# Kernel optimization log

Hardware: AMD Instinct MI355X
Metric: run time of the kernel (lower is better)

The kernel has to match this reference:

```python
import jax, jax.numpy as jnp
import numpy as np

B, S, E, H, VS, VT = 128, 256, 512, 512, 32000, 32000


def _lstm_layer(x, mask, Wih, Whh, bih, bhh):
    # x: (S,B,E_in), mask: (S,B) bool. PyTorch gate order i,f,g,o.
    h0 = jnp.zeros((x.shape[1], Whh.shape[1]), x.dtype)
    c0 = h0
    def step(carry, inp):
        h, c = carry
        xt, mt = inp
        g = xt @ Wih.T + h @ Whh.T + bih + bhh
        i, f, gg, o = jnp.split(g, 4, axis=-1)
        i = jax.nn.sigmoid(i); f = jax.nn.sigmoid(f)
        gg = jnp.tanh(gg); o = jax.nn.sigmoid(o)
        c_new = f * c + i * gg
        h_new = o * jnp.tanh(c_new)
        m = mt[:, None]
        h2 = jnp.where(m, h_new, h)
        c2 = jnp.where(m, c_new, c)
        return (h2, c2), jnp.where(m, h_new, 0.0)  # pad_packed zero-pads
    (hT, cT), ys = jax.lax.scan(step, (h0, c0), (x, mask))
    return ys, cT


def setup_inputs() -> dict:
    key = jax.random.key(0)
    ks = jax.random.split(key, 32)
    def w(k, shape, fan_in):
        bound = 1.0 / np.sqrt(fan_in)
        return jax.random.uniform(k, shape, jnp.float32, -bound, bound)
    src_tokens = jax.random.randint(ks[0], (B, S), 0, VS)
    src_lens = jnp.sort(jax.random.randint(ks[1], (B,), S // 2, S + 1))[::-1]
    src_lens = src_lens.at[0].set(S)  # pack_padded expects descending, max = S
    trg_tokens = jax.random.randint(ks[2], (B,), 0, VT)
    inp = {
        'src_tokens': src_tokens, 'src_lens': src_lens, 'trg_tokens': trg_tokens,
        'src_emb': jax.random.normal(ks[3], (VS, E), jnp.float32),
        'trg_emb': jax.random.normal(ks[4], (VT, E), jnp.float32),
        'enc_Wih0': w(ks[5], (4 * H, E), H), 'enc_Whh0': w(ks[6], (4 * H, H), H),
        'enc_bih0': w(ks[7], (4 * H,), H), 'enc_bhh0': w(ks[8], (4 * H,), H),
        'enc_Wih1': w(ks[9], (4 * H, H), H), 'enc_Whh1': w(ks[10], (4 * H, H), H),
        'enc_bih1': w(ks[11], (4 * H,), H), 'enc_bhh1': w(ks[12], (4 * H,), H),
        'dec_Wih': w(ks[13], (4 * H, E + H), H), 'dec_Whh': w(ks[14], (4 * H, H), H),
        'dec_bih': w(ks[15], (4 * H,), H), 'dec_bhh': w(ks[16], (4 * H,), H),
        'W_init': w(ks[17], (H, 2 * H), 2 * H), 'b_init': w(ks[18], (H,), 2 * H),
        'W_hid': w(ks[19], (H, 2 * H), 2 * H), 'b_hid': w(ks[20], (H,), 2 * H),
        'W_out': w(ks[21], (VT, H), H), 'b_out': w(ks[22], (VT,), H),
    }
    return inp


def reference(src_tokens, src_lens, trg_tokens, src_emb, trg_emb,
              enc_Wih0, enc_Whh0, enc_bih0, enc_bhh0,
              enc_Wih1, enc_Whh1, enc_bih1, enc_bhh1,
              dec_Wih, dec_Whh, dec_bih, dec_bhh,
              W_init, b_init, W_hid, b_hid, W_out, b_out):
    # ---- encode ----
    x = src_emb[src_tokens]                       # (B,S,E)
    x = jnp.transpose(x, (1, 0, 2))               # (S,B,E)
    mask = jnp.arange(S)[:, None] < src_lens[None, :]  # (S,B)
    y0, c0f = _lstm_layer(x, mask, enc_Wih0, enc_Whh0, enc_bih0, enc_bhh0)
    y1, c1f = _lstm_layer(y0, mask, enc_Wih1, enc_Whh1, enc_bih1, enc_bhh1)
    src_states = jnp.transpose(y1, (1, 0, 2))     # (B,S,H)
    # final cell states (num_layers,B,H) -> (B, num_layers*H)
    final_cells = jnp.concatenate([c0f, c1f], axis=-1)  # (B,2H)
    c_dec = final_cells @ W_init.T + b_init       # (B,H)
    h_dec = jnp.tanh(c_dec)
    # ---- one decoder step ----
    emb_t = trg_emb[trg_tokens]                   # (B,E)
    vec = jnp.concatenate([emb_t, jnp.zeros((B, H), emb_t.dtype)], axis=-1)
    g = vec @ dec_Wih.T + h_dec @ dec_Whh.T + dec_bih + dec_bhh
    i, f, gg, o = jnp.split(g, 4, axis=-1)
    c = jax.nn.sigmoid(f) * c_dec + jax.nn.sigmoid(i) * jnp.tanh(gg)
    h = jax.nn.sigmoid(o) * jnp.tanh(c)           # (B,H)
    # ---- masked dot attention ----
    scores = jnp.einsum('bsh,bh->bs', src_states, h)
    smask = jnp.arange(S)[None, :] < src_lens[:, None]
    scores = jnp.where(smask, scores, -jnp.inf)
    attw = jax.nn.softmax(scores, axis=-1)
    context = jnp.einsum('bs,bsh->bh', attw, src_states)
    attn_vec = jnp.concatenate([h, context], axis=-1) @ W_hid.T + b_hid
    logits = attn_vec @ W_out.T + b_out
    prd_token = jnp.argmax(logits, axis=-1)       # softmax is monotone
    return context, h, prd_token
```

## Files before the change

kernel.cpp:

```cpp
#include <hip/hip_runtime.h>
#include <stdint.h>


typedef _Float16 f16;
typedef f16 f16x8 __attribute__((ext_vector_type(8)));
typedef float f32x4 __attribute__((ext_vector_type(4)));

#define LOSCALE 2048.0f
#define LOINV   (1.0f/2048.0f)

#define B_  128
#define S_  256
#define H_  512

__device__ __forceinline__ uint16_t hbits(f16 h){ union{ f16 f; uint16_t u; } c; c.f=h; return c.u; }

__device__ __forceinline__ uint32_t split_ph2(float x){
  f16 h = (f16)x;
  float r = (x - (float)h) * LOSCALE;
  return (uint32_t)hbits(h) | ((uint32_t)hbits((f16)r) << 16);
}
__device__ __forceinline__ float ph2val(uint32_t p){
  union{ uint16_t u; f16 f; } a, b; a.u = (uint16_t)p; b.u = (uint16_t)(p>>16);
  return (float)a.f + (float)b.f * LOINV;
}

__device__ __forceinline__ void pack_hi_lo(const uint4& a, const uint4& b, uint4& hi, uint4& lo){
  hi = make_uint4((a.x & 0xffffu) | (a.y << 16),
                  (a.z & 0xffffu) | (a.w << 16),
                  (b.x & 0xffffu) | (b.y << 16),
                  (b.z & 0xffffu) | (b.w << 16));
  lo = make_uint4((a.x >> 16) | (a.y & 0xffff0000u),
                  (a.z >> 16) | (a.w & 0xffff0000u),
                  (b.x >> 16) | (b.y & 0xffff0000u),
                  (b.z >> 16) | (b.w & 0xffff0000u));
}

__device__ __forceinline__ void split_pack8(const float* x, uint4& hi, uint4& lo){
  uint16_t h[8], l[8];
#pragma unroll
  for (int e = 0; e < 8; ++e) {
    f16 hh = (f16)x[e];
    float r = (x[e] - (float)hh) * LOSCALE;
    h[e] = hbits(hh); l[e] = hbits((f16)r);
  }
  hi = make_uint4((uint32_t)h[0]|((uint32_t)h[1]<<16), (uint32_t)h[2]|((uint32_t)h[3]<<16),
                  (uint32_t)h[4]|((uint32_t)h[5]<<16), (uint32_t)h[6]|((uint32_t)h[7]<<16));
  lo = make_uint4((uint32_t)l[0]|((uint32_t)l[1]<<16), (uint32_t)l[2]|((uint32_t)l[3]<<16),
                  (uint32_t)l[4]|((uint32_t)l[5]<<16), (uint32_t)l[6]|((uint32_t)l[7]<<16));
}

__device__ __forceinline__ f32x4 mfma16(uint4 a, uint4 b, f32x4 c){
  return __builtin_amdgcn_mfma_f32_16x16x32_f16(
      __builtin_bit_cast(f16x8, a), __builtin_bit_cast(f16x8, b), c, 0, 0, 0);
}

__device__ __forceinline__ float sigm(float x){ return 1.0f/(1.0f + expf(-x)); }
__device__ __forceinline__ float fsigm(float x){ return 1.0f/(1.0f + __expf(-x)); }
__device__ __forceinline__ float ftanh(float x){
  float ax = fabsf(x);
  float e = __expf(-2.0f*ax);
  float r = (1.0f - e)/(1.0f + e);
  return copysignf(r, x);
}

__device__ __forceinline__ uint32_t plane_word(uint32_t p, uint32_t pp, int odd){
  return odd ? ((pp >> 16) | (p & 0xffff0000u))
             : ((p & 0xffffu) | (pp << 16));
}

__device__ __forceinline__ size_t fl_idx(int row, int k){
  return (size_t)(k >> 5) * 4096 + (size_t)(row >> 4) * 512 + (size_t)(k & 1) * 256
       + (size_t)((k >> 3) & 3) * 64 + (size_t)(row & 15) * 4 + (size_t)((k & 7) >> 1);
}

__device__ __forceinline__ void gload_lds16(const uint32_t* gbase, uint32_t* lbase, int lane){
#if __has_builtin(__builtin_amdgcn_global_load_lds)
  __builtin_amdgcn_global_load_lds(
      (const __attribute__((address_space(1))) uint32_t*)(gbase + lane*4),
      (__attribute__((address_space(3))) uint32_t*)lbase, 16, 0, 0);
#else
  *(uint4*)(lbase + lane*4) = *(const uint4*)(gbase + lane*4);
#endif
}

__global__ __launch_bounds__(256) void k_embed_src_fl(const int* __restrict__ tok,
    const float* __restrict__ emb, uint32_t* __restrict__ out)
{
  const size_t total = (size_t)S_ * B_ * H_;
  for (size_t i = (size_t)blockIdx.x*256 + threadIdx.x; i < total; i += (size_t)gridDim.x*256) {
    int s = (int)(i >> 16), b = (int)((i >> 9) & 127), k = (int)(i & 511);
    int t = tok[b*S_ + s];
    uint32_t p = split_ph2(emb[(size_t)t*H_ + k]);
    uint32_t pp = __shfl_xor(p, 1);
    out[(size_t)s*65536 + fl_idx(b, k)] = plane_word(p, pp, k & 1);
  }
}

__global__ __launch_bounds__(256) void k_embed_trg(const int* __restrict__ tok,
    const float* __restrict__ emb, uint32_t* __restrict__ out)
{
  int i = blockIdx.x*256 + threadIdx.x;
  int e = i & (H_-1), b = i >> 9;
  int t = tok[b];
  out[i] = split_ph2(emb[(size_t)t*H_ + e]);
}

__global__ __launch_bounds__(256) void k_packW(const float* __restrict__ W,
    uint32_t* __restrict__ out)
{
  int i = blockIdx.x*256 + threadIdx.x;
  int n = i >> 9, k = i & 511;
  uint32_t p = split_ph2(W[i]);
  uint32_t pp = __shfl_xor(p, 1);
  out[(size_t)(n >> 7)*65536 + fl_idx(n & 127, k)] = plane_word(p, pp, k & 1);
}

__global__ __launch_bounds__(256) void k_packAfl(const float* __restrict__ a,
    uint32_t* __restrict__ out)
{
  int i = blockIdx.x*256 + threadIdx.x;
  int b = i >> 9, k = i & 511;
  uint32_t p = split_ph2(a[i]);
  uint32_t pp = __shfl_xor(p, 1);
  out[fl_idx(b, k)] = plane_word(p, pp, k & 1);
}

__global__ __launch_bounds__(256,2) void k_gemm_fl(
    const uint32_t* __restrict__ Afl,
    const uint32_t* __restrict__ Wfl,
    const float* __restrict__ b0, const float* __restrict__ b1,
    float* __restrict__ C, int N, int addC)
{
  __shared__ uint8_t sm[65536];
  const int tid = threadIdx.x, lane = tid & 63, wv = tid >> 6;
  const int wm = wv >> 1, wn = wv & 1;
  const int bn0 = blockIdx.x * 128, bm0 = blockIdx.y * 128;
  const uint32_t* Ab = Afl + (size_t)blockIdx.y * 65536;
  const uint32_t* Wb = Wfl + (size_t)blockIdx.x * 65536;

  f32x4 acc0[4][4], acc1[4][4];
#pragma unroll
  for (int i = 0; i < 4; ++i)
#pragma unroll
    for (int j = 0; j < 4; ++j) { acc0[i][j] = (f32x4){0,0,0,0}; acc1[i][j] = (f32x4){0,0,0,0}; }

  for (int it = 0; it < 8; ++it) {
    __syncthreads();
    {
      const uint32_t* gsrc = (wv < 2 ? Ab : Wb) + (size_t)it*8192 + (size_t)(wv & 1)*4096;
      uint32_t* lb = (uint32_t*)(sm + (size_t)wv*16384);
#pragma unroll
      for (int e = 0; e < 16; ++e)
        gload_lds16(gsrc + e*256, lb + e*256, lane);
    }
    asm volatile("s_waitcnt vmcnt(0)" ::: "memory");
    __syncthreads();

#pragma unroll
    for (int kt = 0; kt < 2; ++kt) {
      uint4 ah[4], al[4];
#pragma unroll
      for (int i = 0; i < 4; ++i) {
        const uint8_t* p = sm + (size_t)(kt*8 + wm*4 + i)*2048 + lane*16;
        ah[i] = *(const uint4*)p; al[i] = *(const uint4*)(p + 1024);
      }
#pragma unroll
      for (int j = 0; j < 4; ++j) {
        const uint8_t* p = sm + 32768 + (size_t)(kt*8 + wn*4 + j)*2048 + lane*16;
        uint4 bh = *(const uint4*)p;
        uint4 bl = *(const uint4*)(p + 1024);
#pragma unroll
        for (int i = 0; i < 4; ++i) {
          acc0[i][j] = mfma16(ah[i], bh, acc0[i][j]);
          acc1[i][j] = mfma16(al[i], bh, acc1[i][j]);
          acc1[i][j] = mfma16(ah[i], bl, acc1[i][j]);
        }
      }
    }
  }

#pragma unroll
  for (int i = 0; i < 4; ++i) {
    int row0 = bm0 + (wm*4+i)*16 + ((lane>>4)<<2);
#pragma unroll
    for (int j = 0; j < 4; ++j) {
      int col = bn0 + (wn*4+j)*16 + (lane & 15);
      float bias = 0.f;
      if (b0) bias += b0[col];
      if (b1) bias += b1[col];
      f32x4 v = acc0[i][j] + acc1[i][j] * LOINV;
#pragma unroll
      for (int r = 0; r < 4; ++r) {
        size_t idx = (size_t)(row0 + r) * N + col;
        float out = v[r] + bias;
        if (addC) out += C[idx];
        C[idx] = out;
      }
    }
  }
}

__global__ __launch_bounds__(256,2) void k_gemm(
    const uint32_t* __restrict__ A, int lda,
    const float* __restrict__ W, int ldw,
    const float* __restrict__ b0, const float* __restrict__ b1,
    float* __restrict__ C, int N, int K, int addC)
{
  __shared__ uint8_t sm[65536];
  const int tid = threadIdx.x;
  const int lane = tid & 63, wv = tid >> 6;
  const int wm = wv >> 1, wn = wv & 1;
  const int bn0 = blockIdx.x * 128, bm0 = blockIdx.y * 128;

  const int srow = tid >> 1;
  const int skh  = (tid & 1) * 32;
  const int smt  = srow >> 4, sr = srow & 15, skt = tid & 1;

  f32x4 acc0[4][4], acc1[4][4];
#pragma unroll
  for (int i = 0; i < 4; ++i)
#pragma unroll
    for (int j = 0; j < 4; ++j) { acc0[i][j] = (f32x4){0,0,0,0}; acc1[i][j] = (f32x4){0,0,0,0}; }

  for (int k0 = 0; k0 < K; k0 += 64) {
    __syncthreads();
    {
      const uint32_t* ap = A + (size_t)(bm0 + srow) * lda + (k0 + skh);
      uint4 q[8];
#pragma unroll
      for (int e = 0; e < 8; ++e) q[e] = *(const uint4*)(ap + e*4);
#pragma unroll
      for (int kg = 0; kg < 4; ++kg) {
        uint4 hi, lo; pack_hi_lo(q[2*kg], q[2*kg+1], hi, lo);
        uint8_t* dst = sm + (size_t)(smt*2 + skt)*2048 + (size_t)(sr + 16*kg)*16;
        *(uint4*)dst = hi; *(uint4*)(dst + 1024) = lo;
      }
    }
    {
      const float* wp = W + (size_t)(bn0 + srow) * ldw + (k0 + skh);
      float xs[32];
#pragma unroll
      for (int e = 0; e < 8; ++e) { float4 v = *(const float4*)(wp + e*4);
        xs[e*4+0]=v.x; xs[e*4+1]=v.y; xs[e*4+2]=v.z; xs[e*4+3]=v.w; }
#pragma unroll
      for (int kg = 0; kg < 4; ++kg) {
        uint4 hi, lo; split_pack8(xs + kg*8, hi, lo);
        uint8_t* dst = sm + 32768 + (size_t)(smt*2 + skt)*2048 + (size_t)(sr + 16*kg)*16;
        *(uint4*)dst = hi; *(uint4*)(dst + 1024) = lo;
      }
    }
    __syncthreads();

#pragma unroll
    for (int kt = 0; kt < 2; ++kt) {
      uint4 ah[4], al[4];
#pragma unroll
      for (int i = 0; i < 4; ++i) {
        const uint8_t* p = sm + (size_t)(((wm*4+i)*2 + kt))*2048 + lane*16;
        ah[i] = *(const uint4*)p; al[i] = *(const uint4*)(p + 1024);
      }
#pragma unroll
      for (int j = 0; j < 4; ++j) {
        const uint8_t* p = sm + 32768 + (size_t)(((wn*4+j)*2 + kt))*2048 + lane*16;
        uint4 bh = *(const uint4*)p;
        uint4 bl = *(const uint4*)(p + 1024);
#pragma unroll
        for (int i = 0; i < 4; ++i) {
          acc0[i][j] = mfma16(ah[i], bh, acc0[i][j]);
          acc1[i][j] = mfma16(al[i], bh, acc1[i][j]);
          acc1[i][j] = mfma16(ah[i], bl, acc1[i][j]);
        }
      }
    }
  }

#pragma unroll
  for (int i = 0; i < 4; ++i) {
    int row0 = bm0 + (wm*4+i)*16 + ((lane>>4)<<2);
#pragma unroll
    for (int j = 0; j < 4; ++j) {
      int col = bn0 + (wn*4+j)*16 + (lane & 15);
      float bias = 0.f;
      if (b0) bias += b0[col];
      if (b1) bias += b1[col];
      f32x4 v = acc0[i][j] + acc1[i][j] * LOINV;
#pragma unroll
      for (int r = 0; r < 4; ++r) {
        size_t idx = (size_t)(row0 + r) * N + col;
        float out = v[r] + bias;
        if (addC) out += C[idx];
        C[idx] = out;
      }
    }
  }
}

__global__ __launch_bounds__(256,1) void k_lstm2(
    const float* __restrict__ Whh0, const float* __restrict__ Whh1,
    const float* __restrict__ bih1, const float* __restrict__ bhh1,
    const float* __restrict__ xg,
    const int*  __restrict__ lens,
    uint32_t* __restrict__ mb0,
    uint32_t* __restrict__ mb1,
    float* __restrict__ cb0, float* __restrict__ cb1,
    uint32_t* __restrict__ y1buf,
    uint32_t* __restrict__ flg0, uint32_t* __restrict__ flg1,
    uint32_t* __restrict__ xcdclaim,
    const uint32_t* __restrict__ Wp1,
    int s0, int nt)
{
  __shared__ uint8_t sm[163840];
  uint8_t* wih = sm;
  uint8_t* tile = sm + 131072;
  uint64_t* tile64 = (uint64_t*)tile;
  float* g0ex = (float*)tile;
  float* g1ex = (float*)(tile + 4096);

  const int tid = threadIdx.x, lane = tid & 63, wv = tid >> 6;
  const int row = lane & 15, qh = lane >> 4;

  uint32_t* claim_sh = (uint32_t*)tile;
  if (tid == 0) {
    uint32_t xcd;
    asm volatile("s_getreg_b32 %0, hwreg(HW_REG_XCC_ID)" : "=s"(xcd));
    xcd &= 7u;
    uint32_t pos = __hip_atomic_fetch_add(xcdclaim + xcd*16, 1u,
                     __ATOMIC_RELAXED, __HIP_MEMORY_SCOPE_SYSTEM);
    claim_sh[0] = xcd | ((pos & 31u) << 8);
  }
  __syncthreads();
  const uint32_t cl = claim_sh[0];
  const int bg = (int)(cl & 7u), hs = (int)((cl >> 8) & 31u);
  __syncthreads();

  {
    const uint32_t* wpb = Wp1 + (size_t)(wv*4 + (hs >> 3))*65536 + (size_t)(hs & 7)*512;
    uint32_t* lb = (uint32_t*)(wih + (size_t)wv*32768);
#pragma unroll
    for (int kt = 0; kt < 16; ++kt) {
      gload_lds16(wpb + kt*4096,       lb + kt*512,       lane);
      gload_lds16(wpb + kt*4096 + 256, lb + kt*512 + 256, lane);
    }
  }

  uint4 w0h[16], w0l[16], w1h[16], w1l[16];
  {
    const float* r0 = Whh0 + (size_t)(wv*512 + hs*16 + row)*512 + qh*8;
    const float* r1 = Whh1 + (size_t)(wv*512 + hs*16 + row)*512 + qh*8;
#pragma unroll
    for (int kt = 0; kt < 16; ++kt) {
      float xs[8];
      float4 v0 = *(const float4*)(r0 + kt*32), v1 = *(const float4*)(r0 + kt*32 + 4);
      xs[0]=v0.x; xs[1]=v0.y; xs[2]=v0.z; xs[3]=v0.w;
      xs[4]=v1.x; xs[5]=v1.y; xs[6]=v1.z; xs[7]=v1.w;
      split_pack8(xs, w0h[kt], w0l[kt]);
      v0 = *(const float4*)(r1 + kt*32); v1 = *(const float4*)(r1 + kt*32 + 4);
      xs[0]=v0.x; xs[1]=v0.y; xs[2]=v0.z; xs[3]=v0.w;
      xs[4]=v1.x; xs[5]=v1.y; xs[6]=v1.z; xs[7]=v1.w;
      split_pack8(xs, w1h[kt], w1l[kt]);
    }
  }

  const int b_l = tid >> 4, uu = tid & 15;
  const int bglob = bg*16 + b_l;
  const size_t bgoff = (size_t)bg*8192;
  const int oct_p = hs*2 + (uu >> 3);
  const size_t widx = (size_t)b_l*512 + (size_t)(uu & 1)*256
                    + ((size_t)(oct_p ^ b_l) << 2) + (size_t)((uu & 7) >> 1);
  const int len_b = lens[bglob];
  const int lenA  = lens[bg*16 + row];
  float c0_reg = cb0[(size_t)bglob*512 + hs*16 + uu];
  float c1_reg = cb1[(size_t)bglob*512 + hs*16 + uu];
  float h0_reg, h1_reg;
  {
    size_t ib = (size_t)(s0 & 1)*65536 + bgoff + (size_t)b_l*512
              + ((size_t)(oct_p ^ b_l) << 2) + (size_t)((uu & 7) >> 1);
    uint32_t hiw = mb0[ib], low = mb0[ib + 256];
    int sh = (uu & 1) * 16;
    union{ uint16_t u; f16 f; } ch, cl2;
    ch.u = (uint16_t)(hiw >> sh); cl2.u = (uint16_t)(low >> sh);
    h0_reg = (float)ch.f + (float)cl2.f * LOINV;
    int s1i = (s0 >= 1) ? (s0 - 1) : 0;
    size_t ib1 = (size_t)(s1i & 1)*65536 + bgoff + (size_t)b_l*512
               + ((size_t)(oct_p ^ b_l) << 2) + (size_t)((uu & 7) >> 1);
    hiw = mb1[ib1]; low = mb1[ib1 + 256];
    ch.u = (uint16_t)(hiw >> sh); cl2.u = (uint16_t)(low >> sh);
    h1_reg = (float)ch.f + (float)cl2.f * LOINV;
  }
  float b1g[4];
#pragma unroll
  for (int g = 0; g < 4; ++g)
    b1g[g] = bih1[g*512 + hs*16 + uu] + bhh1[g*512 + hs*16 + uu];
  const size_t yfl = (size_t)(hs >> 1)*4096 + (size_t)bg*512 + (size_t)(uu & 1)*256
                   + (size_t)((((hs & 1) << 1) | (uu >> 3)))*64 + (size_t)b_l*4
                   + (size_t)((uu & 7) >> 1);

  asm volatile("s_waitcnt vmcnt(0)" ::: "memory");
  __syncthreads();

  for (int it = 0; it < nt; ++it) {
    const int t = s0 + it;
    const bool aL0 = (t < 256);
    const bool aL1 = (t > 0);

    float xv0 = 0.f, xv1 = 0.f, xv2 = 0.f, xv3 = 0.f;
    if (aL0) {
      const float* xgp = xg + ((size_t)it*128 + bglob)*2048 + hs*16 + uu;
      xv0 = xgp[0]; xv1 = xgp[512]; xv2 = xgp[1024]; xv3 = xgp[1536];
    }

    if (it > 0) {
      if (wv == 0) {
        const uint32_t* fp = flg0 + bg*32 + (lane & 31);
        while (1) {
          uint32_t f = __hip_atomic_load(fp, __ATOMIC_RELAXED, __HIP_MEMORY_SCOPE_AGENT);
          if (__all((int)(f >= (uint32_t)t))) break;
          __builtin_amdgcn_s_sleep(1);
        }
      } else if (wv == 1) {
        const uint32_t* fp = flg1 + bg*32 + (lane & 31);
        while (1) {
          uint32_t f = __hip_atomic_load(fp, __ATOMIC_RELAXED, __HIP_MEMORY_SCOPE_AGENT);
          if (__all((int)(f >= (uint32_t)(t - 1)))) break;
          __builtin_amdgcn_s_sleep(1);
        }
      }
    }
    __builtin_amdgcn_s_barrier();
    __builtin_amdgcn_sched_barrier(0);

    const uint64_t* sp0 = (const uint64_t*)(mb0 + (size_t)(t & 1)*65536 + bgoff);
    const uint64_t* sp1 = (const uint64_t*)(mb1 + (size_t)((t - 1) & 1)*65536 + bgoff);
    uint64_t v0[16], v1[16];
#pragma unroll
    for (int e = 0; e < 16; ++e)
      v0[e] = __hip_atomic_load(sp0 + tid + e*256, __ATOMIC_RELAXED, __HIP_MEMORY_SCOPE_AGENT);
    if (aL1) {
#pragma unroll
      for (int e = 0; e < 16; ++e)
        v1[e] = __hip_atomic_load(sp1 + tid + e*256, __ATOMIC_RELAXED, __HIP_MEMORY_SCOPE_AGENT);
    }
#pragma unroll
    for (int e = 0; e < 16; ++e)
      tile64[tid + e*256] = v0[e];
    asm volatile("s_waitcnt lgkmcnt(0)" ::: "memory");
    __builtin_amdgcn_s_barrier();
    __builtin_amdgcn_sched_barrier(0);

    f32x4 A0 = (f32x4){0,0,0,0}, A1 = (f32x4){0,0,0,0}, A2 = (f32x4){0,0,0,0};
    f32x4 B0 = (f32x4){0,0,0,0}, B1 = (f32x4){0,0,0,0}, B2 = (f32x4){0,0,0,0};
    {
      const uint8_t* hrp = tile + (size_t)row*2048;
      const uint8_t* wbase = wih + (size_t)wv*32768;
      const bool cY = aL1 && ((t - 1) < lenA);
      const uint4 z4 = make_uint4(0,0,0,0);
#pragma unroll
      for (int kt = 0; kt < 16; ++kt) {
        int oct = kt*4 + qh;
        const uint8_t* pA = hrp + (((oct ^ row)) << 4);
        uint4 ah = *(const uint4*)pA, al = *(const uint4*)(pA + 1024);
        A0 = mfma16(ah, w0h[kt], A0);
        A1 = mfma16(al, w0h[kt], A1);
        A2 = mfma16(ah, w0l[kt], A2);
        uint4 yh = cY ? ah : z4, yl = cY ? al : z4;
        const uint8_t* pB = wbase + (size_t)kt*2048 + lane*16;
        uint4 bh = *(const uint4*)pB, bl = *(const uint4*)(pB + 1024);
        B0 = mfma16(yh, bh, B0);
        B1 = mfma16(yl, bh, B1);
        B2 = mfma16(yh, bl, B2);
      }
    }
    __builtin_amdgcn_sched_barrier(0);
    __builtin_amdgcn_s_barrier();
    __builtin_amdgcn_sched_barrier(0);

    if (aL1) {
#pragma unroll
      for (int e = 0; e < 16; ++e)
        tile64[tid + e*256] = v1[e];
    }
    asm volatile("s_waitcnt lgkmcnt(0)" ::: "memory");
    __builtin_amdgcn_s_barrier();
    __builtin_amdgcn_sched_barrier(0);

    if (aL1) {
      const uint8_t* hrp = tile + (size_t)row*2048;
#pragma unroll
      for (int kt = 0; kt < 16; ++kt) {
        int oct = kt*4 + qh;
        const uint8_t* pA = hrp + (((oct ^ row)) << 4);
        uint4 ah = *(const uint4*)pA, al = *(const uint4*)(pA + 1024);
        B0 = mfma16(ah, w1h[kt], B0);
        B1 = mfma16(al, w1h[kt], B1);
        B2 = mfma16(ah, w1l[kt], B2);
      }
    }
    __builtin_amdgcn_sched_barrier(0);
    __builtin_amdgcn_s_barrier();
    __builtin_amdgcn_sched_barrier(0);

    {
      int col = lane & 15, rb = (lane >> 4) << 2;
      if (aL0) {
#pragma unroll
        for (int r = 0; r < 4; ++r)
          g0ex[(size_t)(wv*16 + rb + r)*16 + col] = A0[r] + (A1[r] + A2[r])*LOINV;
      }
      if (aL1) {
#pragma unroll
        for (int r = 0; r < 4; ++r)
          g1ex[(size_t)(wv*16 + rb + r)*16 + col] = B0[r] + (B1[r] + B2[r])*LOINV;
      }
    }
    asm volatile("s_waitcnt lgkmcnt(0)" ::: "memory");
    __builtin_amdgcn_s_barrier();
    __builtin_amdgcn_sched_barrier(0);

    uint32_t p1w = 0; bool m1 = false;
    if (aL0) {
      float gi = g0ex[(size_t)(0*16 + b_l)*16 + uu] + xv0;
      float gf = g0ex[(size_t)(1*16 + b_l)*16 + uu] + xv1;
      float gg = g0ex[(size_t)(2*16 + b_l)*16 + uu] + xv2;
      float go = g0ex[(size_t)(3*16 + b_l)*16 + uu] + xv3;
      float cn = fsigm(gf)*c0_reg + fsigm(gi)*ftanh(gg);
      float hn = fsigm(go)*ftanh(cn);
      bool m = (t < len_b);
      c0_reg = m ? cn : c0_reg;
      h0_reg = m ? hn : h0_reg;
      uint32_t p = split_ph2(h0_reg);
      uint32_t pp = __shfl_xor(p, 1);
      __hip_atomic_store(mb0 + (size_t)((t + 1) & 1)*65536 + bgoff + widx,
                         plane_word(p, pp, uu & 1), __ATOMIC_RELAXED, __HIP_MEMORY_SCOPE_AGENT);
    }
    if (aL1) {
      float gi = g1ex[(size_t)(0*16 + b_l)*16 + uu] + b1g[0];
      float gf = g1ex[(size_t)(1*16 + b_l)*16 + uu] + b1g[1];
      float gg = g1ex[(size_t)(2*16 + b_l)*16 + uu] + b1g[2];
      float go = g1ex[(size_t)(3*16 + b_l)*16 + uu] + b1g[3];
      float cn = fsigm(gf)*c1_reg + fsigm(gi)*ftanh(gg);
      float hn = fsigm(go)*ftanh(cn);
      m1 = ((t - 1) < len_b);
      c1_reg = m1 ? cn : c1_reg;
      h1_reg = m1 ? hn : h1_reg;
      uint32_t p = split_ph2(h1_reg);
      uint32_t pp = __shfl_xor(p, 1);
      p1w = plane_word(p, pp, uu & 1);
      __hip_atomic_store(mb1 + (size_t)(t & 1)*65536 + bgoff + widx,
                         p1w, __ATOMIC_RELAXED, __HIP_MEMORY_SCOPE_AGENT);
    }
    asm volatile("s_waitcnt vmcnt(0)" ::: "memory");
    __builtin_amdgcn_s_barrier();
    __builtin_amdgcn_sched_barrier(0);
    if (tid == 0) {
      if (aL0) __hip_atomic_store(flg0 + bg*32 + hs, (uint32_t)(t + 1),
                                  __ATOMIC_RELAXED, __HIP_MEMORY_SCOPE_AGENT);
      if (aL1) __hip_atomic_store(flg1 + bg*32 + hs, (uint32_t)t,
                                  __ATOMIC_RELAXED, __HIP_MEMORY_SCOPE_AGENT);
    }
    if (aL1) y1buf[(size_t)(t - 1)*65536 + yfl] = m1 ? p1w : 0u;
  }
  cb0[(size_t)bglob*512 + hs*16 + uu] = c0_reg;
  cb1[(size_t)bglob*512 + hs*16 + uu] = c1_reg;
}

__global__ __launch_bounds__(256) void k_pack2(const float* __restrict__ a,
    const float* __restrict__ b, uint32_t* __restrict__ out)
{
  int i = blockIdx.x*256 + threadIdx.x;
  int bb = i >> 10, k = i & 1023;
  float x = (k < 512) ? a[(size_t)bb*512 + k] : b[(size_t)bb*512 + k - 512];
  out[i] = split_ph2(x);
}

__global__ __launch_bounds__(256) void k_tanh_split(const float* __restrict__ c,
    uint32_t* __restrict__ hp)
{ int i = blockIdx.x*256 + threadIdx.x; hp[i] = split_ph2(tanhf(c[i])); }

__global__ __launch_bounds__(256) void k_dec_cell(const float* __restrict__ g,
    const float* __restrict__ cdec, float* __restrict__ hout, float* __restrict__ dh)
{
  int i = blockIdx.x*256 + threadIdx.x;
  int b = i >> 9, u = i & 511;
  const float* gb = g + (size_t)b*2048;
  float c = sigm(gb[512 + u])*cdec[i] + sigm(gb[u])*tanhf(gb[1024 + u]);
  float h = sigm(gb[1536 + u])*tanhf(c);
  hout[i] = h; dh[i] = h;
}

__global__ __launch_bounds__(256) void k_attn(const uint32_t* __restrict__ y1,
    const float* __restrict__ h, const int* __restrict__ lens,
    float* __restrict__ ctx, float* __restrict__ dctx)
{
  __shared__ float hsh[512];
  __shared__ float sc[256];
  __shared__ float red[8];
  const int b = blockIdx.x, tid = threadIdx.x, lane = tid & 63, wv = tid >> 6;
  hsh[tid]       = h[(size_t)b*512 + tid];
  hsh[tid + 256] = h[(size_t)b*512 + tid + 256];
  const int len = lens[b];
  __syncthreads();

  const size_t lanebase = (size_t)(lane >> 2)*4096 + (size_t)(b >> 4)*512
                        + (size_t)(lane & 3)*64 + (size_t)(b & 15)*4;
  for (int it = 0; it < 64; ++it) {
    int s = wv*64 + it;
    const uint32_t* yb = y1 + (size_t)s*65536 + lanebase;
    uint4 hw = *(const uint4*)yb;
    uint4 lw = *(const uint4*)(yb + 256);
    int k0 = lane*8;
    uint32_t hws[4] = {hw.x,hw.y,hw.z,hw.w}, lws[4] = {lw.x,lw.y,lw.z,lw.w};
    float d = 0.f;
#pragma unroll
    for (int w = 0; w < 4; ++w) {
      union{uint16_t u; f16 f;} h0,h1,l0,l1;
      h0.u=(uint16_t)hws[w]; h1.u=(uint16_t)(hws[w]>>16);
      l0.u=(uint16_t)lws[w]; l1.u=(uint16_t)(lws[w]>>16);
      d += ((float)h0.f + (float)l0.f*LOINV) * hsh[k0 + 2*w]
         + ((float)h1.f + (float)l1.f*LOINV) * hsh[k0 + 2*w + 1];
    }
    for (int off = 32; off; off >>= 1) d += __shfl_xor(d, off);
    if (lane == 0) sc[s] = d;
  }
  __syncthreads();

  float v = (tid < len) ? sc[tid] : -INFINITY;
  float mx = v;
  for (int off = 32; off; off >>= 1) mx = fmaxf(mx, __shfl_xor(mx, off));
  if (lane == 0) red[wv] = mx;
  __syncthreads();
  mx = fmaxf(fmaxf(red[0], red[1]), fmaxf(red[2], red[3]));
  float e = (tid < len) ? expf(v - mx) : 0.f;
  float ssum = e;
  for (int off = 32; off; off >>= 1) ssum += __shfl_xor(ssum, off);
  if (lane == 0) red[4 + wv] = ssum;
  __syncthreads();
  float tot = red[4] + red[5] + red[6] + red[7];
  __syncthreads();
  sc[tid] = e / tot;
  __syncthreads();

  const int u0 = tid, u1 = tid + 256;
  const size_t bu0 = (size_t)(u0 >> 5)*4096 + (size_t)(b >> 4)*512
                   + (size_t)((u0 >> 3) & 3)*64 + (size_t)(b & 15)*4 + (size_t)((u0 & 7) >> 1);
  const size_t bu1 = (size_t)(u1 >> 5)*4096 + (size_t)(b >> 4)*512
                   + (size_t)((u1 >> 3) & 3)*64 + (size_t)(b & 15)*4 + (size_t)((u1 & 7) >> 1);
  const int sh = (tid & 1) * 16;
  float acc0 = 0.f, acc1 = 0.f;
  for (int s = 0; s < 256; ++s) {
    float w = sc[s];
    const uint32_t* yb = y1 + (size_t)s*65536;
    uint32_t hi0 = yb[bu0], lo0 = yb[bu0 + 256];
    uint32_t hi1 = yb[bu1], lo1 = yb[bu1 + 256];
    union{uint16_t u; f16 f;} a,b2,c2,d2;
    a.u =(uint16_t)(hi0 >> sh); b2.u=(uint16_t)(lo0 >> sh);
    c2.u=(uint16_t)(hi1 >> sh); d2.u=(uint16_t)(lo1 >> sh);
    acc0 += w*((float)a.f  + (float)b2.f*LOINV);
    acc1 += w*((float)c2.f + (float)d2.f*LOINV);
  }
  ctx [(size_t)b*512 + tid]       = acc0;  ctx [(size_t)b*512 + tid + 256] = acc1;
  dctx[(size_t)b*512 + tid]       = acc0;  dctx[(size_t)b*512 + tid + 256] = acc1;
}

__global__ __launch_bounds__(256) void k_argmax(const float* __restrict__ logits,
    float* __restrict__ out)
{
  __shared__ float bv[256];
  __shared__ int   bi[256];
  const int b = blockIdx.x, tid = threadIdx.x;
  const float* L = logits + (size_t)b*32000;
  float best = -INFINITY; int idx = 0;
  for (int i = tid; i < 32000; i += 256) {
    float v = L[i];
    if (v > best) { best = v; idx = i; }
  }
  bv[tid] = best; bi[tid] = idx;
  __syncthreads();
  for (int sft = 128; sft; sft >>= 1) {
    if (tid < sft) {
      if (bv[tid+sft] > bv[tid] || (bv[tid+sft] == bv[tid] && bi[tid+sft] < bi[tid])) {
        bv[tid] = bv[tid+sft]; bi[tid] = bi[tid+sft];
      }
    }
    __syncthreads();
  }
  if (tid == 0) out[b] = (float)bi[0];
}

extern "C" void kernel_launch(void* const* d_in, const int* in_sizes, int n_in,
                              void* d_out, int out_size, void* d_ws, size_t ws_size,
                              hipStream_t stream)
{
  (void)in_sizes; (void)n_in; (void)out_size; (void)ws_size;
  const int*   src_tokens = (const int*)  d_in[0];
  const int*   src_lens   = (const int*)  d_in[1];
  const int*   trg_tokens = (const int*)  d_in[2];
  const float* src_emb    = (const float*)d_in[3];
  const float* trg_emb    = (const float*)d_in[4];
  const float* Wih0 = (const float*)d_in[5];
  const float* Whh0 = (const float*)d_in[6];
  const float* bih0 = (const float*)d_in[7];
  const float* bhh0 = (const float*)d_in[8];
  const float* Wih1 = (const float*)d_in[9];
  const float* Whh1 = (const float*)d_in[10];
  const float* bih1 = (const float*)d_in[11];
  const float* bhh1 = (const float*)d_in[12];
  const float* dWih = (const float*)d_in[13];
  const float* dWhh = (const float*)d_in[14];
  const float* dbih = (const float*)d_in[15];
  const float* dbhh = (const float*)d_in[16];
  const float* Winit= (const float*)d_in[17];
  const float* binit= (const float*)d_in[18];
  const float* Whid = (const float*)d_in[19];
  const float* bhid = (const float*)d_in[20];
  const float* Wout = (const float*)d_in[21];
  const float* bout = (const float*)d_in[22];

  uint8_t* ws = (uint8_t*)d_ws;
  constexpr size_t MBs = 1ull << 20;
  constexpr size_t OFF_AP    = 0;
  constexpr size_t OFF_Y1    = 64*MBs;
  constexpr size_t OFF_XG    = 128*MBs;
  constexpr size_t OFF_MB    = 192*MBs;
  constexpr size_t OFF_CB0   = OFF_MB    + 1*MBs;
  constexpr size_t OFF_CB1   = OFF_CB0   + 256*1024;
  constexpr size_t OFF_FLG   = OFF_CB1   + 256*1024;
  constexpr size_t OFF_PK    = OFF_FLG   + 4096;
  constexpr size_t OFF_CDEC  = OFF_PK    + 512*1024;
  constexpr size_t OFF_HDECP = OFF_CDEC  + 256*1024;
  constexpr size_t OFF_EMBP  = OFF_HDECP + 256*1024;
  constexpr size_t OFF_G     = OFF_EMBP  + 256*1024;
  constexpr size_t OFF_HDEC2 = OFF_G     + 1*MBs;
  constexpr size_t OFF_CTX   = OFF_HDEC2 + 256*1024;
  constexpr size_t OFF_AVEC  = OFF_CTX   + 256*1024;
  constexpr size_t OFF_AVECP = OFF_AVEC  + 256*1024;
  constexpr size_t OFF_LOG   = OFF_AVECP + 256*1024;

  uint32_t* Ap    = (uint32_t*)(ws + OFF_AP);
  uint32_t* Y1    = (uint32_t*)(ws + OFF_Y1);
  float*    Xg    = (float*)   (ws + OFF_XG);
  uint32_t* WoutF = (uint32_t*)(ws + OFF_XG);
  uint32_t* mb0   = (uint32_t*)(ws + OFF_MB);
  uint32_t* mb1   = (uint32_t*)(ws + OFF_MB + 512*1024);
  float*    cb0   = (float*)   (ws + OFF_CB0);
  float*    cb1   = (float*)   (ws + OFF_CB1);
  uint32_t* flg0  = (uint32_t*)(ws + OFF_FLG);
  uint32_t* xclm  = (uint32_t*)(ws + OFF_FLG + 1024);
  uint32_t* flg1  = (uint32_t*)(ws + OFF_FLG + 2048);
  uint32_t* pk    = (uint32_t*)(ws + OFF_PK);
  float*    cdec  = (float*)   (ws + OFF_CDEC);
  uint32_t* hdecp = (uint32_t*)(ws + OFF_HDECP);
  uint32_t* embp  = (uint32_t*)(ws + OFF_EMBP);
  float*    g     = (float*)   (ws + OFF_G);
  float*    hdec2 = (float*)   (ws + OFF_HDEC2);
  float*    ctx   = (float*)   (ws + OFF_CTX);
  float*    avec  = (float*)   (ws + OFF_AVEC);
  uint32_t* avecp = (uint32_t*)(ws + OFF_AVECP);
  float*    logit = (float*)   (ws + OFF_LOG);
  uint32_t* Wp0   = (uint32_t*)(ws + OFF_LOG);
  uint32_t* Wp1   = (uint32_t*)(ws + OFF_LOG + 4*MBs);
  float*    dout  = (float*)   d_out;

  k_packW<<<4096, 256, 0, stream>>>(Wih0, Wp0);
  k_packW<<<4096, 256, 0, stream>>>(Wih1, Wp1);

  hipMemsetAsync(mb0,  0, 1024*1024, stream);
  hipMemsetAsync(flg0, 0, 4096, stream);
  hipMemsetAsync(cb0,  0, 65536*4, stream);
  hipMemsetAsync(cb1,  0, 65536*4, stream);
  k_embed_src_fl<<<2048, 256, 0, stream>>>(src_tokens, src_emb, Ap);
  for (int c = 0; c < 4; ++c) {
    int s0 = c * 64;
    k_gemm_fl<<<dim3(16, 64), 256, 0, stream>>>(Ap + (size_t)s0*65536,
        Wp0, bih0, bhh0, Xg, 2048, 0);
    k_lstm2<<<256, 256, 0, stream>>>(Whh0, Whh1, bih1, bhh1, Xg, src_lens,
        mb0, mb1, cb0, cb1, Y1, flg0, flg1, xclm, Wp1, s0, (c == 3) ? 65 : 64);
  }

  k_packW<<<64000, 256, 0, stream>>>(Wout, WoutF);

  k_pack2<<<512, 256, 0, stream>>>(cb0, cb1, pk);
  k_gemm<<<dim3(4, 1), 256, 0, stream>>>(pk, 1024, Winit, 1024, binit, nullptr,
      cdec, 512, 1024, 0);
  k_tanh_split<<<256, 256, 0, stream>>>(cdec, hdecp);

  k_embed_trg<<<256, 256, 0, stream>>>(trg_tokens, trg_emb, embp);
  k_gemm<<<dim3(16, 1), 256, 0, stream>>>(embp, 512, dWih, 1024, dbih, dbhh,
      g, 2048, 512, 0);
  k_gemm<<<dim3(16, 1), 256, 0, stream>>>(hdecp, 512, dWhh, 512, nullptr, nullptr,
      g, 2048, 512, 1);
  k_dec_cell<<<256, 256, 0, stream>>>(g, cdec, hdec2, dout + 65536);

  k_attn<<<128, 256, 0, stream>>>(Y1, hdec2, src_lens, ctx, dout);

  k_pack2<<<512, 256, 0, stream>>>(hdec2, ctx, pk);
  k_gemm<<<dim3(4, 1), 256, 0, stream>>>(pk, 1024, Whid, 1024, bhid, nullptr,
      avec, 512, 1024, 0);
  k_packAfl<<<256, 256, 0, stream>>>(avec, avecp);
  k_gemm_fl<<<dim3(250, 1), 256, 0, stream>>>(avecp, WoutF, bout, nullptr,
      logit, 32000, 0);
  k_argmax<<<128, 256, 0, stream>>>(logit, dout + 131072);
}
```

Measured before the change: 2.501 ms.

## Double-buffer layer tiles and drop low-part Wih1 MFMA to remove barriers

The single shared h tile becomes two separate tiles for layer 0 and layer 1, so both hidden states are staged together and two block barriers per timestep go away. The layer-1 input weight staged in LDS keeps only its high fp16 half, which halves that LDS footprint and drops one MFMA per k-step in the input projection. This lowers per-step sync and compute on the serial recurrence critical path. The risk is lower precision in the layer-1 input projection, since the weight low-part correction term is no longer applied.

```diff
diff --git a/kernel.cpp b/kernel.cpp
--- a/kernel.cpp
+++ b/kernel.cpp
@@ -310,17 +310,19 @@
     const uint32_t* __restrict__ Wp1,
     int s0, int nt)
 {
-  __shared__ uint8_t sm[163840];
-  uint8_t* wih = sm;
-  uint8_t* tile = sm + 131072;
-  uint64_t* tile64 = (uint64_t*)tile;
-  float* g0ex = (float*)tile;
-  float* g1ex = (float*)(tile + 4096);
+  __shared__ uint8_t sm[139264];
+  uint8_t* wih   = sm;
+  uint8_t* tileA = sm + 65536;
+  uint8_t* tileB = sm + 98304;
+  uint64_t* tA64 = (uint64_t*)tileA;
+  uint64_t* tB64 = (uint64_t*)tileB;
+  float* g0ex = (float*)(sm + 131072);
+  float* g1ex = (float*)(sm + 135168);
 
   const int tid = threadIdx.x, lane = tid & 63, wv = tid >> 6;
   const int row = lane & 15, qh = lane >> 4;
 
-  uint32_t* claim_sh = (uint32_t*)tile;
+  uint32_t* claim_sh = (uint32_t*)tileA;
   if (tid == 0) {
     uint32_t xcd;
     asm volatile("s_getreg_b32 %0, hwreg(HW_REG_XCC_ID)" : "=s"(xcd));
@@ -336,12 +338,10 @@
 
   {
     const uint32_t* wpb = Wp1 + (size_t)(wv*4 + (hs >> 3))*65536 + (size_t)(hs & 7)*512;
-    uint32_t* lb = (uint32_t*)(wih + (size_t)wv*32768);
-#pragma unroll
-    for (int kt = 0; kt < 16; ++kt) {
-      gload_lds16(wpb + kt*4096,       lb + kt*512,       lane);
-      gload_lds16(wpb + kt*4096 + 256, lb + kt*512 + 256, lane);
-    }
+    uint32_t* lb = (uint32_t*)(wih + (size_t)wv*16384);
+#pragma unroll
+    for (int kt = 0; kt < 16; ++kt)
+      gload_lds16(wpb + kt*4096, lb + kt*256, lane);
   }
 
   uint4 w0h[16], w0l[16], w1h[16], w1l[16];
@@ -430,20 +430,27 @@
     __builtin_amdgcn_s_barrier();
     __builtin_amdgcn_sched_barrier(0);
 
-    const uint64_t* sp0 = (const uint64_t*)(mb0 + (size_t)(t & 1)*65536 + bgoff);
-    const uint64_t* sp1 = (const uint64_t*)(mb1 + (size_t)((t - 1) & 1)*65536 + bgoff);
-    uint64_t v0[16], v1[16];
-#pragma unroll
-    for (int e = 0; e < 16; ++e)
-      v0[e] = __hip_atomic_load(sp0 + tid + e*256, __ATOMIC_RELAXED, __HIP_MEMORY_SCOPE_AGENT);
-    if (aL1) {
+    {
+      const uint64_t* sp0 = (const uint64_t*)(mb0 + (size_t)(t & 1)*65536 + bgoff);
+      const uint64_t* sp1 = (const uint64_t*)(mb1 + (size_t)((t - 1) & 1)*65536 + bgoff);
+      uint64_t v0[16], v1[16];
 #pragma unroll
       for (int e = 0; e < 16; ++e)
-        v1[e] = __hip_atomic_load(sp1 + tid + e*256, __ATOMIC_RELAXED, __HIP_MEMORY_SCOPE_AGENT);
-    }
-#pragma unroll
-    for (int e = 0; e < 16; ++e)
-      tile64[tid + e*256] = v0[e];
+        v0[e] = __hip_atomic_load(sp0 + tid + e*256, __ATOMIC_RELAXED, __HIP_MEMORY_SCOPE_AGENT);
+      if (aL1) {
+#pragma unroll
+        for (int e = 0; e < 16; ++e)
+          v1[e] = __hip_atomic_load(sp1 + tid + e*256, __ATOMIC_RELAXED, __HIP_MEMORY_SCOPE_AGENT);
+      }
+#pragma unroll
+      for (int e = 0; e < 16; ++e)
+        tA64[tid + e*256] = v0[e];
+      if (aL1) {
+#pragma unroll
+        for (int e = 0; e < 16; ++e)
+          tB64[tid + e*256] = v1[e];
+      }
+    }
     asm volatile("s_waitcnt lgkmcnt(0)" ::: "memory");
     __builtin_amdgcn_s_barrier();
     __builtin_amdgcn_sched_barrier(0);
@@ -451,8 +458,8 @@
     f32x4 A0 = (f32x4){0,0,0,0}, A1 = (f32x4){0,0,0,0}, A2 = (f32x4){0,0,0,0};
     f32x4 B0 = (f32x4){0,0,0,0}, B1 = (f32x4){0,0,0,0}, B2 = (f32x4){0,0,0,0};
     {
-      const uint8_t* hrp = tile + (size_t)row*2048;
-      const uint8_t* wbase = wih + (size_t)wv*32768;
+      const uint8_t* hrp = tileA + (size_t)row*2048;
+      const uint8_t* wbase = wih + (size_t)wv*16384;
       const bool cY = aL1 && ((t - 1) < lenA);
       const uint4 z4 = make_uint4(0,0,0,0);
 #pragma unroll
@@ -464,28 +471,13 @@
         A1 = mfma16(al, w0h[kt], A1);
         A2 = mfma16(ah, w0l[kt], A2);
         uint4 yh = cY ? ah : z4, yl = cY ? al : z4;
-        const uint8_t* pB = wbase + (size_t)kt*2048 + lane*16;
-        uint4 bh = *(const uint4*)pB, bl = *(const uint4*)(pB + 1024);
+        uint4 bh = *(const uint4*)(wbase + (size_t)kt*1024 + lane*16);
         B0 = mfma16(yh, bh, B0);
         B1 = mfma16(yl, bh, B1);
-        B2 = mfma16(yh, bl, B2);
-      }
-    }
-    __builtin_amdgcn_sched_barrier(0);
-    __builtin_amdgcn_s_barrier();
-    __builtin_amdgcn_sched_barrier(0);
-
+      }
+    }
     if (aL1) {
-#pragma unroll
-      for (int e = 0; e < 16; ++e)
-        tile64[tid + e*256] = v1[e];
-    }
-    asm volatile("s_waitcnt lgkmcnt(0)" ::: "memory");
-    __builtin_amdgcn_s_barrier();
-    __builtin_amdgcn_sched_barrier(0);
-
-    if (aL1) {
-      const uint8_t* hrp = tile + (size_t)row*2048;
+      const uint8_t* hrp = tileB + (size_t)row*2048;
 #pragma unroll
       for (int kt = 0; kt < 16; ++kt) {
         int oct = kt*4 + qh;
@@ -496,9 +488,6 @@
         B2 = mfma16(ah, w1l[kt], B2);
       }
     }
-    __builtin_amdgcn_sched_barrier(0);
-    __builtin_amdgcn_s_barrier();
-    __builtin_amdgcn_sched_barrier(0);
 
     {
       int col = lane & 15, rb = (lane >> 4) << 2;
```

Measured after the change: 2.409 ms. 1.04x faster.
